# Kernel optimization log

Measured on AMD Instinct MI355X. Metric: run time of the kernel, lower is better.

## Reference

```python
import jax, jax.numpy as jnp
import numpy as np

IN_FEATURES = 4096
OUT_FEATURES = 4096
RANK = 16
TOKENS = 8192


def setup_inputs() -> dict:
    key = jax.random.key(0)
    k1, k2, k3, k4, k5 = jax.random.split(key, 5)
    x = jax.random.normal(k1, (TOKENS, IN_FEATURES), dtype=jnp.float32)
    orig_weight = jax.random.normal(k2, (IN_FEATURES, OUT_FEATURES), dtype=jnp.float32) * 0.02
    lora_u = jax.random.normal(k3, (IN_FEATURES, RANK), dtype=jnp.float32) * 0.02
    lora_s = jax.random.uniform(k4, (RANK,), dtype=jnp.float32)
    lora_vt = jax.random.normal(k5, (RANK, OUT_FEATURES), dtype=jnp.float32) * 0.02
    return {"x": x, "orig_weight": orig_weight, "lora_u": lora_u,
            "lora_s": lora_s, "lora_vt": lora_vt}


def reference(x, orig_weight, lora_u, lora_s, lora_vt):
    # Faithful to torch: W = orig_weight + lora_u @ diag(lora_s) @ lora_vt; out = x @ W
    # diag(s) contraction expressed as a column scale of lora_u (same math).
    delta = (lora_u * lora_s[None, :]) @ lora_vt  # [in, out] low-rank delta
    return x @ (orig_weight + delta)
```

## Files before the change

### kernel.cpp

```cpp
#include <hip/hip_runtime.h>
#include <hip/hip_bf16.h>
#include <stdint.h>

#define TOKENS 8192
#define NF 4096
#define KF 4096
#define RANK 16

typedef __attribute__((ext_vector_type(8))) short bf16x8;
typedef __attribute__((ext_vector_type(4))) float f32x4;
typedef __attribute__((ext_vector_type(8))) unsigned short u16x8;

static __device__ __forceinline__ unsigned short f2b(float f) {
    union { float f; uint32_t u; } v; v.f = f;
    uint32_t u = v.u;
    uint32_t r = (u + 0x7fffu + ((u >> 16) & 1u)) >> 16;
    return (unsigned short)r;
}

__global__ __launch_bounds__(256) void prep_w_kernel(
    const float* __restrict__ W, const float* __restrict__ U,
    const float* __restrict__ s, const float* __restrict__ Vt,
    unsigned short* __restrict__ Wt)
{
    __shared__ float Us[64][16];
    __shared__ float Vs[16][64];
    __shared__ float tile[64][65];
    const int kb = blockIdx.x, nb = blockIdx.y;
    const int t = threadIdx.x;
    for (int idx = t; idx < 64 * 16; idx += 256) {
        int kl = idx >> 4, r = idx & 15;
        Us[kl][r] = U[(size_t)(kb * 64 + kl) * RANK + r];
    }
    for (int idx = t; idx < 16 * 64; idx += 256) {
        int r = idx >> 6, nl = idx & 63;
        Vs[r][nl] = Vt[(size_t)r * NF + nb * 64 + nl] * s[r];
    }
    __syncthreads();
    const int nl = t & 63, kl0 = t >> 6;
    for (int i = 0; i < 16; ++i) {
        int kl = kl0 + i * 4;
        float v = __builtin_nontemporal_load(&W[(size_t)(kb * 64 + kl) * NF + nb * 64 + nl]);
        #pragma unroll
        for (int r = 0; r < RANK; ++r) v += Us[kl][r] * Vs[r][nl];
        tile[kl][nl] = v;
    }
    __syncthreads();
    #pragma unroll
    for (int j = 0; j < 2; ++j) {
        int idx = t + j * 256;
        int kg = idx & 7, n = idx >> 3;
        u16x8 o;
        #pragma unroll
        for (int e = 0; e < 8; ++e) o[e] = f2b(tile[kg * 8 + e][n]);
        *(u16x8*)&Wt[(size_t)(nb * 64 + n) * KF + kb * 64 + kg * 8] = o;
    }
}

__global__ __launch_bounds__(256) void prep_x_kernel(
    const float* __restrict__ x, unsigned short* __restrict__ xb)
{
    size_t base = ((size_t)blockIdx.x * 256 + threadIdx.x) * 8;
    f32x4 a = __builtin_nontemporal_load((const f32x4*)(x + base));
    f32x4 b = __builtin_nontemporal_load((const f32x4*)(x + base + 4));
    u16x8 o;
    o[0] = f2b(a[0]); o[1] = f2b(a[1]); o[2] = f2b(a[2]); o[3] = f2b(a[3]);
    o[4] = f2b(b[0]); o[5] = f2b(b[1]); o[6] = f2b(b[2]); o[7] = f2b(b[3]);
    *(u16x8*)(xb + base) = o;
}


#define VM4  asm volatile("s_waitcnt vmcnt(4)" ::: "memory")

#define MFMA(a, b, c) __builtin_amdgcn_mfma_f32_16x16x32_bf16(a, b, c, 0, 0, 0)

#define LDA4(dn, qn, afr) do {                                                  \
    afr[0] = ldA(dn, 2*(qn), 0);   afr[1] = ldA(dn, 2*(qn), 1);                 \
    afr[2] = ldA(dn, 2*(qn)+1, 0); afr[3] = ldA(dn, 2*(qn)+1, 1);               \
} while (0)

#define LDB_ALL(d, bfr) do {                                                    \
    _Pragma("unroll")                                                           \
    for (int nf = 0; nf < 4; ++nf) {                                            \
        bfr[nf][0] = ldB(d, nf, 0);                                             \
        bfr[nf][1] = ldB(d, nf, 1);                                             \
    } } while (0)

#define MFMA16(q, bfr, afr) do {                                                \
    _Pragma("unroll")                                                           \
    for (int nf = 0; nf < 4; ++nf) {                                            \
        acc[2*(q)][nf]   = MFMA(afr[0], bfr[nf][0], acc[2*(q)][nf]);            \
        acc[2*(q)][nf]   = MFMA(afr[1], bfr[nf][1], acc[2*(q)][nf]);            \
        acc[2*(q)+1][nf] = MFMA(afr[2], bfr[nf][0], acc[2*(q)+1][nf]);          \
        acc[2*(q)+1][nf] = MFMA(afr[3], bfr[nf][1], acc[2*(q)+1][nf]);          \
    } } while (0)

#define PHASE(q, bfr, afrC, dn, qn, afrN, STAGE_EXPR) do {                      \
    STAGE_EXPR;                                                                 \
    __builtin_amdgcn_s_barrier();                                               \
    asm volatile("s_waitcnt lgkmcnt(0)" ::: "memory");                          \
    __builtin_amdgcn_s_setprio(1);                                              \
    LDA4(dn, qn, afrN);                                                         \
    MFMA16(q, bfr, afrC);                                                       \
    __builtin_amdgcn_s_setprio(0);                                              \
} while (0)

#define PHASEX(q, bfr, afrC, dn, qn, afrN, bnxt, dnb, STAGE_EXPR) do {          \
    STAGE_EXPR;                                                                 \
    VM4;                                                                        \
    __builtin_amdgcn_s_barrier();                                               \
    asm volatile("s_waitcnt lgkmcnt(0)" ::: "memory");                          \
    __builtin_amdgcn_s_setprio(1);                                              \
    LDB_ALL(dnb, bnxt);                                                         \
    LDA4(dn, qn, afrN);                                                         \
    MFMA16(q, bfr, afrC);                                                       \
    __builtin_amdgcn_s_setprio(0);                                              \
} while (0)

__global__ __launch_bounds__(512, 2) void gemm_kernel(
    const unsigned short* __restrict__ A,
    const unsigned short* __restrict__ Bt,
    float* __restrict__ C)
{
    __shared__ __align__(16) unsigned short lds[65536];

    const int tid  = threadIdx.x;
    const int lane = tid & 63;
    const int wave = tid >> 6;
    const int wm = wave >> 2;
    const int wn = wave & 3;

    const int bid = blockIdx.x;
    const int swz = (bid & 7) * 64 + (bid >> 3);
    const int tm = swz >> 4;
    const int tn = swz & 15;

    const int frow = lane & 15;
    const int kgrp = lane >> 4;
    const int xorv = (frow & 7) << 4;

    const int st_row  = tid >> 3;
    const int st_colE = ((((tid & 7) * 16) ^ (((tid >> 3) & 7) << 4)) >> 1);
    const unsigned short* aSrc = A  + (size_t)(tm * 256 + st_row) * KF + st_colE;
    const unsigned short* bSrc = Bt + (size_t)(tn * 256 + st_row) * KF + st_colE;
    const int dstE = tid * 8;

    f32x4 acc[8][4] = {};

    auto stage = [&](int isB, int d, int h, int kt) {
        const unsigned short* src =
            (isB ? bSrc : aSrc) + (size_t)((h) * 128) * KF + (kt) * 64;
        unsigned short* dst = (unsigned short*)&lds[isB * 32768 + (d * 2 + h) * 8192 + dstE];
        __builtin_amdgcn_global_load_lds(
            (const __attribute__((address_space(1))) void*)src,
            (__attribute__((address_space(3))) void*)dst, 16, 0, 0);
        __builtin_amdgcn_global_load_lds(
            (const __attribute__((address_space(1))) void*)(src + (size_t)64 * KF),
            (__attribute__((address_space(3))) void*)(dst + 4096), 16, 0, 0);
    };

    auto ldA = [&](int d, int mf, int kk) -> bf16x8 {
        int off = (d * 2 + wm) * 8192 + (mf * 16 + frow) * 64
                + ((((kk << 6) | (kgrp << 4)) ^ xorv) >> 1);
        return *(const bf16x8*)&lds[off];
    };
    auto ldB = [&](int d, int nf, int kk) -> bf16x8 {
        int off = 32768 + (d * 2 + (wn >> 1)) * 8192
                + ((wn & 1) * 64 + nf * 16 + frow) * 64
                + ((((kk << 6) | (kgrp << 4)) ^ xorv) >> 1);
        return *(const bf16x8*)&lds[off];
    };

    bf16x8 bfrP[4][2], bfrQ[4][2];
    bf16x8 afrP[4], afrQ[4];

    stage(1, 0, 0, 0); stage(1, 0, 1, 0);
    stage(0, 0, 0, 0); stage(0, 0, 1, 0);
    stage(1, 1, 0, 1); stage(1, 1, 1, 1);
    VM4;
    __builtin_amdgcn_s_barrier();
    asm volatile("" ::: "memory");
    LDB_ALL(0, bfrP);
    LDA4(0, 0, afrP);

    for (int i = 0; i < 32; ++i) {
        const int kt1 = 2 * i + 1;
        const int kt2 = (2 * i + 2) & 63;
        const int kt3 = (2 * i + 3) & 63;

        PHASE (0, bfrP, afrP, 0, 1, afrQ, stage(0, 1, 0, kt1));
        PHASE (1, bfrP, afrQ, 0, 2, afrP, stage(0, 1, 1, kt1));
        PHASE (2, bfrP, afrP, 0, 3, afrQ, stage(1, 0, 0, kt2));
        PHASEX(3, bfrP, afrQ, 1, 0, afrP, bfrQ, 1, stage(1, 0, 1, kt2));
        PHASE (0, bfrQ, afrP, 1, 1, afrQ, stage(0, 0, 0, kt2));
        PHASE (1, bfrQ, afrQ, 1, 2, afrP, stage(0, 0, 1, kt2));
        PHASE (2, bfrQ, afrP, 1, 3, afrQ, stage(1, 1, 0, kt3));
        PHASEX(3, bfrQ, afrQ, 0, 0, afrP, bfrP, 0, stage(1, 1, 1, kt3));
    }

    asm volatile("s_waitcnt vmcnt(0)" ::: "memory");

    const int rgrp = lane >> 4, coll = lane & 15;
    #pragma unroll
    for (int mf = 0; mf < 8; ++mf)
        #pragma unroll
        for (int nf = 0; nf < 4; ++nf) {
            size_t row0 = (size_t)(tm * 256 + wm * 128 + mf * 16 + rgrp * 4);
            size_t col  = (size_t)(tn * 256 + wn * 64 + nf * 16 + coll);
            #pragma unroll
            for (int r = 0; r < 4; ++r)
                C[(row0 + r) * NF + col] = acc[mf][nf][r];
        }
}

extern "C" void kernel_launch(void* const* d_in, const int* in_sizes, int n_in,
                              void* d_out, int out_size, void* d_ws, size_t ws_size,
                              hipStream_t stream) {
    const float* x  = (const float*)d_in[0];
    const float* W  = (const float*)d_in[1];
    const float* U  = (const float*)d_in[2];
    const float* s  = (const float*)d_in[3];
    const float* Vt = (const float*)d_in[4];
    float* out = (float*)d_out;

    unsigned short* Wt = (unsigned short*)d_ws;
    unsigned short* xb = Wt + (size_t)NF * KF;

    prep_w_kernel<<<dim3(KF / 64, NF / 64), 256, 0, stream>>>(W, U, s, Vt, Wt);
    prep_x_kernel<<<(TOKENS * KF / 8) / 256, 256, 0, stream>>>(x, xb);
    gemm_kernel<<<(TOKENS / 256) * (NF / 256), 512, 0, stream>>>(xb, Wt, out);
}
```

Measured before the change: 286.1 us.

## Merge GEMM main-loop phases into four per iteration and drop A-fragment prefetch

Restructures the main loop from eight barrier-separated phases to four per iteration. Each phase now loads eight A fragments from LDS and immediately issues 32 MFMAs, instead of prefetching the next phase's A fragments into a ping-pong register pair. The explicit lgkmcnt(0) wait before the MFMA block is replaced by a compiler memory fence, and each phase issues two global-to-LDS stage calls. This halves the barrier count and frees A-fragment registers, but LDS read latency is no longer hidden behind the previous phase's MFMAs.

```diff
diff --git a/kernel.cpp b/kernel.cpp
--- a/kernel.cpp
+++ b/kernel.cpp
@@ -74,10 +74,12 @@
 
 #define MFMA(a, b, c) __builtin_amdgcn_mfma_f32_16x16x32_bf16(a, b, c, 0, 0, 0)
 
-#define LDA4(dn, qn, afr) do {                                                  \
-    afr[0] = ldA(dn, 2*(qn), 0);   afr[1] = ldA(dn, 2*(qn), 1);                 \
-    afr[2] = ldA(dn, 2*(qn)+1, 0); afr[3] = ldA(dn, 2*(qn)+1, 1);               \
-} while (0)
+#define LDA8(dn, qh, afr) do {                                                  \
+    _Pragma("unroll")                                                           \
+    for (int j = 0; j < 4; ++j) {                                               \
+        afr[2*j]   = ldA(dn, 4*(qh) + j, 0);                                    \
+        afr[2*j+1] = ldA(dn, 4*(qh) + j, 1);                                    \
+    } } while (0)
 
 #define LDB_ALL(d, bfr) do {                                                    \
     _Pragma("unroll")                                                           \
@@ -86,34 +88,34 @@
         bfr[nf][1] = ldB(d, nf, 1);                                             \
     } } while (0)
 
-#define MFMA16(q, bfr, afr) do {                                                \
+#define MFMA32(qh, bfr, afr) do {                                               \
     _Pragma("unroll")                                                           \
-    for (int nf = 0; nf < 4; ++nf) {                                            \
-        acc[2*(q)][nf]   = MFMA(afr[0], bfr[nf][0], acc[2*(q)][nf]);            \
-        acc[2*(q)][nf]   = MFMA(afr[1], bfr[nf][1], acc[2*(q)][nf]);            \
-        acc[2*(q)+1][nf] = MFMA(afr[2], bfr[nf][0], acc[2*(q)+1][nf]);          \
-        acc[2*(q)+1][nf] = MFMA(afr[3], bfr[nf][1], acc[2*(q)+1][nf]);          \
-    } } while (0)
-
-#define PHASE(q, bfr, afrC, dn, qn, afrN, STAGE_EXPR) do {                      \
+    for (int j = 0; j < 4; ++j)                                                 \
+        _Pragma("unroll")                                                       \
+        for (int nf = 0; nf < 4; ++nf) {                                        \
+            acc[4*(qh)+j][nf] = MFMA(afr[2*j],   bfr[nf][0], acc[4*(qh)+j][nf]);\
+            acc[4*(qh)+j][nf] = MFMA(afr[2*j+1], bfr[nf][1], acc[4*(qh)+j][nf]);\
+        } } while (0)
+
+#define PHASE4(dc, qh, bfr, STAGE_EXPR) do {                                    \
     STAGE_EXPR;                                                                 \
     __builtin_amdgcn_s_barrier();                                               \
-    asm volatile("s_waitcnt lgkmcnt(0)" ::: "memory");                          \
+    asm volatile("" ::: "memory");                                              \
     __builtin_amdgcn_s_setprio(1);                                              \
-    LDA4(dn, qn, afrN);                                                         \
-    MFMA16(q, bfr, afrC);                                                       \
+    LDA8(dc, qh, afr);                                                          \
+    MFMA32(qh, bfr, afr);                                                       \
     __builtin_amdgcn_s_setprio(0);                                              \
 } while (0)
 
-#define PHASEX(q, bfr, afrC, dn, qn, afrN, bnxt, dnb, STAGE_EXPR) do {          \
+#define PHASE4X(dc, qh, bfr, bnxt, dnb, STAGE_EXPR) do {                        \
     STAGE_EXPR;                                                                 \
     VM4;                                                                        \
     __builtin_amdgcn_s_barrier();                                               \
-    asm volatile("s_waitcnt lgkmcnt(0)" ::: "memory");                          \
+    asm volatile("" ::: "memory");                                              \
     __builtin_amdgcn_s_setprio(1);                                              \
     LDB_ALL(dnb, bnxt);                                                         \
-    LDA4(dn, qn, afrN);                                                         \
-    MFMA16(q, bfr, afrC);                                                       \
+    LDA8(dc, qh, afr);                                                          \
+    MFMA32(qh, bfr, afr);                                                       \
     __builtin_amdgcn_s_setprio(0);                                              \
 } while (0)
 
@@ -172,7 +174,7 @@
     };
 
     bf16x8 bfrP[4][2], bfrQ[4][2];
-    bf16x8 afrP[4], afrQ[4];
+    bf16x8 afr[8];
 
     stage(1, 0, 0, 0); stage(1, 0, 1, 0);
     stage(0, 0, 0, 0); stage(0, 0, 1, 0);
@@ -181,21 +183,16 @@
     __builtin_amdgcn_s_barrier();
     asm volatile("" ::: "memory");
     LDB_ALL(0, bfrP);
-    LDA4(0, 0, afrP);
 
     for (int i = 0; i < 32; ++i) {
         const int kt1 = 2 * i + 1;
         const int kt2 = (2 * i + 2) & 63;
         const int kt3 = (2 * i + 3) & 63;
 
-        PHASE (0, bfrP, afrP, 0, 1, afrQ, stage(0, 1, 0, kt1));
-        PHASE (1, bfrP, afrQ, 0, 2, afrP, stage(0, 1, 1, kt1));
-        PHASE (2, bfrP, afrP, 0, 3, afrQ, stage(1, 0, 0, kt2));
-        PHASEX(3, bfrP, afrQ, 1, 0, afrP, bfrQ, 1, stage(1, 0, 1, kt2));
-        PHASE (0, bfrQ, afrP, 1, 1, afrQ, stage(0, 0, 0, kt2));
-        PHASE (1, bfrQ, afrQ, 1, 2, afrP, stage(0, 0, 1, kt2));
-        PHASE (2, bfrQ, afrP, 1, 3, afrQ, stage(1, 1, 0, kt3));
-        PHASEX(3, bfrQ, afrQ, 0, 0, afrP, bfrP, 0, stage(1, 1, 1, kt3));
+        PHASE4 (0, 0, bfrP, (stage(0, 1, 0, kt1), stage(0, 1, 1, kt1)));
+        PHASE4X(0, 1, bfrP, bfrQ, 1, (stage(1, 0, 0, kt2), stage(1, 0, 1, kt2)));
+        PHASE4 (1, 0, bfrQ, (stage(0, 0, 0, kt2), stage(0, 0, 1, kt2)));
+        PHASE4X(1, 1, bfrQ, bfrP, 0, (stage(1, 1, 0, kt3), stage(1, 1, 1, kt3)));
     }
 
     asm volatile("s_waitcnt vmcnt(0)" ::: "memory");
```

Result: no change. 289.2 us (+1.1%).
